# Kernel optimization log

Hardware: AMD Instinct MI355X
Metric: run time of the kernel (lower is better)

## Reference

```python
import jax, jax.numpy as jnp
import numpy as np

EPS = 1e-4          # module eps
GROUPS = 8
N_POWER_ITERS = 19  # fixed iteration count for power_iteration_unstable


def _l2n(v):
    return v / (jnp.linalg.norm(v) + 1e-12)


def _whiten_subspace(A, v_init):
    """Sequential power iteration + deflation on one LxL covariance block.
    A: (L, L), v_init: (L, L) random start vectors (one per eigen-index).
    Returns whitening subspace (L, L). Early-exit (break) emulated with a
    'stopped' flag carried through lax.scan."""
    L = A.shape[0]

    def step(carry, inputs):
        A, subspace, lam_prev, stopped = carry
        j, v0 = inputs
        v = _l2n(v0)

        def pi(v, _):
            return _l2n(A @ v), None
        v, _ = jax.lax.scan(pi, v, None, length=N_POWER_ITERS)

        Av = A @ v
        lam = (v @ Av) / (v @ v)          # Rayleigh quotient
        brk = (j > 0) & ((lam_prev < lam) | (lam < EPS))  # torch break condition
        active = (~stopped) & (~brk)
        lam_safe = jnp.where(active, lam, 1.0)
        vvT = jnp.outer(v, v)
        subspace = subspace + jnp.where(active, jax.lax.rsqrt(lam_safe), 0.0) * vvT
        A = jnp.where(active, A - A @ vvT, A)
        lam_prev = jnp.where(active, lam, lam_prev)
        stopped = stopped | brk
        return (A, subspace, lam_prev, stopped), None

    init = (A, jnp.zeros_like(A), jnp.zeros((), A.dtype), jnp.zeros((), bool))
    (_, subspace, _, _), _ = jax.lax.scan(step, init, (jnp.arange(L), v_init))
    return subspace


def setup_inputs() -> dict:
    key = jax.random.key(0)
    k1, k2, k3 = jax.random.split(key, 3)
    N, C, H, W = 32, 512, 56, 56
    L = C // GROUPS
    x = jax.random.normal(k1, (N, C, H, W), dtype=jnp.float32)
    v_init = jax.random.normal(k2, (GROUPS, L, L), dtype=jnp.float32)
    weight = jax.random.uniform(k3, (C, 1), dtype=jnp.float32)
    bias = jnp.zeros((C, 1), dtype=jnp.float32)
    return {"x": x, "v_init": v_init, "weight": weight, "bias": bias}


def reference(x, v_init, weight, bias):
    N, C, H, W = x.shape
    G = GROUPS
    L = C // G
    M = N * H * W
    xc = x.transpose(1, 0, 2, 3).reshape(C, M)        # (C, M)
    mu = xc.mean(axis=1, keepdims=True)
    xc = xc - mu
    xg = xc.reshape(G, L, M)                           # per-group channels
    # diagonal blocks of (x x^T)/M + eps*I
    cov = jnp.einsum('gim,gjm->gij', xg, xg) / M + EPS * jnp.eye(L, dtype=xc.dtype)
    subspaces = jax.vmap(_whiten_subspace)(cov, v_init)  # (G, L, L)
    xgr = jnp.einsum('gij,gjm->gim', subspaces, xg)      # whitened
    xr = xgr.reshape(C, M) * weight + bias               # affine
    return xr.reshape(C, N, H, W).transpose(1, 0, 2, 3)
```

## Files before the change

kernel.cpp:

```cpp
#include <hip/hip_runtime.h>
#include <math.h>

#define EPSV 1e-4f
#define NG 8
#define LL 64
#define NB 32
#define CC 512
#define HWS 3136
#define MTOT (NB * HWS)
#define NPI 19
#define NTILES 49
#define NPW 4

template <int CTRL>
__device__ __forceinline__ float dpp_add(float v) {
  int x = __builtin_amdgcn_update_dpp(0, __float_as_int(v), CTRL, 0xF, 0xF, true);
  return v + __int_as_float(x);
}

__device__ __forceinline__ float wave_allsum(float v) {
  v = dpp_add<0xB1>(v);
  v = dpp_add<0x4E>(v);
  v = dpp_add<0x141>(v);
  v = dpp_add<0x140>(v);
  v += __int_as_float(__builtin_amdgcn_ds_swizzle(__float_as_int(v), 0x401F));
  v += __shfl_xor(v, 32, 64);
  return v;
}

__global__ __launch_bounds__(256, 2) void k_moments(const float* __restrict__ x,
                                                    float* __restrict__ prods,
                                                    float* __restrict__ sums,
                                                    int nparts) {
  const int g = blockIdx.x, n = blockIdx.y, h = blockIdx.z;
  const int tid = threadIdx.x;
  const int q = tid >> 6, l = tid & 63;
  const int ty = tid >> 4, tx = tid & 15;
  __shared__ float xs[64][68];
  const float* xp = x + ((size_t)(n * CC + g * LL)) * HWS;

  float acc[4][4];
#pragma unroll
  for (int a = 0; a < 4; ++a)
#pragma unroll
    for (int b = 0; b < 4; ++b) acc[a][b] = 0.f;
  float csum[16];
#pragma unroll
  for (int r = 0; r < 16; ++r) csum[r] = 0.f;

  const int tpp = (NTILES + nparts - 1) / nparts;
  const int t0 = h * tpp;
  const int t1 = (t0 + tpp < NTILES) ? (t0 + tpp) : NTILES;

  for (int t = t0; t < t1; ++t) {
    const int hw0 = t * 64;
    __syncthreads();
#pragma unroll
    for (int r = 0; r < 16; ++r) {
      const int ch = r * 4 + q;
      float v = xp[ch * HWS + hw0 + l];
      xs[l][ch] = v;
      csum[r] += v;
    }
    __syncthreads();
#pragma unroll 4
    for (int mm = 0; mm < 64; ++mm) {
      const float4* row = (const float4*)(&xs[mm][0]);
      float4 av = row[ty];
      float4 bv = row[tx];
      float a4[4] = {av.x, av.y, av.z, av.w};
      float b4[4] = {bv.x, bv.y, bv.z, bv.w};
#pragma unroll
      for (int ii = 0; ii < 4; ++ii)
#pragma unroll
        for (int jj = 0; jj < 4; ++jj) acc[ii][jj] += a4[ii] * b4[jj];
    }
  }

  const int p = n * nparts + h;
  float* pp = prods + ((size_t)(g * NB * nparts + p)) * 4096;
#pragma unroll
  for (int ii = 0; ii < 4; ++ii) {
    *(float4*)&pp[(ty * 4 + ii) * 64 + tx * 4] =
        make_float4(acc[ii][0], acc[ii][1], acc[ii][2], acc[ii][3]);
  }
#pragma unroll
  for (int r = 0; r < 16; ++r) {
    float s = wave_allsum(csum[r]);
    if (l == 0) sums[((size_t)(g * NB * nparts + p)) * 64 + r * 4 + q] = s;
  }
}

__global__ __launch_bounds__(64) void k_mu(const float* __restrict__ sums,
                                           float* __restrict__ mu, int P) {
  const int g = blockIdx.x;
  const int tid = threadIdx.x;
  const float* sp = sums + (size_t)g * P * 64 + tid;
  float s0 = 0.f, s1 = 0.f, s2 = 0.f, s3 = 0.f;
  int p = 0;
  for (; p + 4 <= P; p += 4) {
    s0 += sp[(size_t)(p + 0) * 64];
    s1 += sp[(size_t)(p + 1) * 64];
    s2 += sp[(size_t)(p + 2) * 64];
    s3 += sp[(size_t)(p + 3) * 64];
  }
  for (; p < P; ++p) s0 += sp[(size_t)p * 64];
  mu[g * 64 + tid] = ((s0 + s1) + (s2 + s3)) / (float)MTOT;
}

__global__ __launch_bounds__(256) void k_cov(const float* __restrict__ prods,
                                             const float* __restrict__ mu,
                                             float* __restrict__ cov, int P) {
  const int g = blockIdx.x;
  const int e = blockIdx.y * 256 + threadIdx.x;
  const int i = e >> 6, j = e & 63;
  const float* pp = prods + (size_t)g * P * 4096 + e;
  float s0 = 0.f, s1 = 0.f, s2 = 0.f, s3 = 0.f;
  int p = 0;
  for (; p + 4 <= P; p += 4) {
    s0 += pp[(size_t)(p + 0) * 4096];
    s1 += pp[(size_t)(p + 1) * 4096];
    s2 += pp[(size_t)(p + 2) * 4096];
    s3 += pp[(size_t)(p + 3) * 4096];
  }
  for (; p < P; ++p) s0 += pp[(size_t)p * 4096];
  const float s = (s0 + s1) + (s2 + s3);
  const float cv =
      s / (float)MTOT - mu[g * 64 + i] * mu[g * 64 + j] + (i == j ? EPSV : 0.f);
  cov[(size_t)g * 4096 + e] = cv;
}

__device__ __forceinline__ float dot64(const float* Arow, const float* v_sh) {
  float d0 = 0.f, d1 = 0.f, d2 = 0.f, d3 = 0.f;
#pragma unroll
  for (int c4 = 0; c4 < 16; ++c4) {
    float4 vv = ((const float4*)v_sh)[c4];
    d0 += Arow[c4 * 4 + 0] * vv.x;
    d1 += Arow[c4 * 4 + 1] * vv.y;
    d2 += Arow[c4 * 4 + 2] * vv.z;
    d3 += Arow[c4 * 4 + 3] * vv.w;
  }
  return (d0 + d1) + (d2 + d3);
}

__global__ __launch_bounds__(64, 1) void k_power(const float* __restrict__ v_init,
                                                 const float* __restrict__ cov,
                                                 float* __restrict__ sub) {
  const int g = blockIdx.x;
  const int r = threadIdx.x;
  __shared__ __align__(16) float v_sh[64];
  float Arow[64], Srow[64];
  const float4* crow = (const float4*)(cov + (size_t)g * 4096 + r * 64);
#pragma unroll
  for (int c4 = 0; c4 < 16; ++c4) {
    float4 cv = crow[c4];
    Arow[c4 * 4 + 0] = cv.x;
    Arow[c4 * 4 + 1] = cv.y;
    Arow[c4 * 4 + 2] = cv.z;
    Arow[c4 * 4 + 3] = cv.w;
    Srow[c4 * 4 + 0] = 0.f;
    Srow[c4 * 4 + 1] = 0.f;
    Srow[c4 * 4 + 2] = 0.f;
    Srow[c4 * 4 + 3] = 0.f;
  }

  float lam_prev = 0.f;
  for (int j = 0; j < 64; ++j) {
    float v0 = v_init[((size_t)g * 64 + j) * 64 + r];
    float ss = wave_allsum(v0 * v0);
    float vr = v0 / (sqrtf(ss) + 1e-12f);
    __syncthreads();
    v_sh[r] = vr;
    __syncthreads();

    for (int it = 0; it < NPI; ++it) {
      float w = dot64(Arow, v_sh);
      float s2 = wave_allsum(w * w);
      vr = w / (sqrtf(s2) + 1e-12f);
      __syncthreads();
      v_sh[r] = vr;
      __syncthreads();
    }

    const float Avr = dot64(Arow, v_sh);
    const float num = wave_allsum(vr * Avr);
    const float den = wave_allsum(vr * vr);
    const float lam = num / den;

    if (j > 0 && (lam_prev < lam || lam < EPSV)) break;

    const float sc = 1.f / sqrtf(lam);
    const float svr = sc * vr;
#pragma unroll
    for (int c4 = 0; c4 < 16; ++c4) {
      float4 vv = ((const float4*)v_sh)[c4];
      Srow[c4 * 4 + 0] += svr * vv.x;
      Srow[c4 * 4 + 1] += svr * vv.y;
      Srow[c4 * 4 + 2] += svr * vv.z;
      Srow[c4 * 4 + 3] += svr * vv.w;
      Arow[c4 * 4 + 0] -= Avr * vv.x;
      Arow[c4 * 4 + 1] -= Avr * vv.y;
      Arow[c4 * 4 + 2] -= Avr * vv.z;
      Arow[c4 * 4 + 3] -= Avr * vv.w;
    }
    lam_prev = lam;
  }

  float4* srow = (float4*)(sub + (size_t)g * 4096 + r * 64);
#pragma unroll
  for (int c4 = 0; c4 < 16; ++c4)
    srow[c4] = make_float4(Srow[c4 * 4 + 0], Srow[c4 * 4 + 1], Srow[c4 * 4 + 2],
                           Srow[c4 * 4 + 3]);
}

__global__ __launch_bounds__(256, 2) void k_whiten(const float* __restrict__ x,
                                                   const float* __restrict__ weight,
                                                   const float* __restrict__ bias,
                                                   const float* __restrict__ mu,
                                                   const float* __restrict__ sub,
                                                   float* __restrict__ out,
                                                   int nparts) {
  const int g = blockIdx.x, n = blockIdx.y, h = blockIdx.z;
  const int tid = threadIdx.x;
  const int q = tid >> 6, l = tid & 63;
  const int ty = tid >> 4, tx = tid & 15;
  __shared__ float xs[64][68];
  __shared__ float ST[64][68];
  __shared__ float mu_sh[64];

  const float* sp = sub + (size_t)g * 4096;
#pragma unroll
  for (int r = 0; r < 16; ++r) {
    const int i = r * 4 + q;
    ST[l][i] = sp[i * 64 + l];
  }
  if (tid < 64) mu_sh[tid] = mu[g * 64 + tid];

  float wgt[4], bs[4];
#pragma unroll
  for (int ii = 0; ii < 4; ++ii) {
    const int cch = g * LL + ty * 4 + ii;
    wgt[ii] = weight[cch];
    bs[ii] = bias[cch];
  }

  const float* xp = x + ((size_t)(n * CC + g * LL)) * HWS;
  float* yp = out + ((size_t)(n * CC + g * LL)) * HWS;
  const int tpp = (NTILES + nparts - 1) / nparts;
  const int t0 = h * tpp;
  const int t1 = (t0 + tpp < NTILES) ? (t0 + tpp) : NTILES;

  __syncthreads();
  for (int t = t0; t < t1; ++t) {
    const int hw0 = t * 64;
    if (t > t0) __syncthreads();
#pragma unroll
    for (int r = 0; r < 16; ++r) {
      const int ch = r * 4 + q;
      xs[ch][l] = xp[ch * HWS + hw0 + l] - mu_sh[ch];
    }
    __syncthreads();

    float acc[4][4];
#pragma unroll
    for (int ii = 0; ii < 4; ++ii)
#pragma unroll
      for (int jj = 0; jj < 4; ++jj) acc[ii][jj] = 0.f;

#pragma unroll 4
    for (int j = 0; j < 64; ++j) {
      float4 sv = ((const float4*)(&ST[j][0]))[ty];
      float4 xv = ((const float4*)(&xs[j][0]))[tx];
      float s4[4] = {sv.x, sv.y, sv.z, sv.w};
      float x4[4] = {xv.x, xv.y, xv.z, xv.w};
#pragma unroll
      for (int ii = 0; ii < 4; ++ii)
#pragma unroll
        for (int jj = 0; jj < 4; ++jj) acc[ii][jj] += s4[ii] * x4[jj];
    }

#pragma unroll
    for (int ii = 0; ii < 4; ++ii) {
      float4 o;
      o.x = acc[ii][0] * wgt[ii] + bs[ii];
      o.y = acc[ii][1] * wgt[ii] + bs[ii];
      o.z = acc[ii][2] * wgt[ii] + bs[ii];
      o.w = acc[ii][3] * wgt[ii] + bs[ii];
      *(float4*)&yp[(ty * 4 + ii) * HWS + hw0 + tx * 4] = o;
    }
  }
}

extern "C" void kernel_launch(void* const* d_in, const int* in_sizes, int n_in,
                              void* d_out, int out_size, void* d_ws, size_t ws_size,
                              hipStream_t stream) {
  const float* x = (const float*)d_in[0];
  const float* v_init = (const float*)d_in[1];
  const float* weight = (const float*)d_in[2];
  const float* bias = (const float*)d_in[3];
  float* out = (float*)d_out;
  float* ws = (float*)d_ws;

  const size_t fixed = (size_t)512 + (size_t)2 * NG * 4096;
  auto need = [&](int np) {
    return ((size_t)NG * NB * np * (4096 + 64) + fixed) * sizeof(float);
  };
  int nparts = 7;
  if (ws_size < need(nparts)) nparts = 4;
  if (ws_size < need(nparts)) nparts = 2;
  if (ws_size < need(nparts)) nparts = 1;

  const int P = NB * nparts;
  float* prods = ws;
  float* sums = prods + (size_t)NG * P * 64;
  sums = prods + (size_t)NG * P * 4096;
  float* mu = sums + (size_t)NG * P * 64;
  float* cov = mu + 512;
  float* sub = cov + (size_t)NG * 4096;

  k_moments<<<dim3(NG, NB, nparts), 256, 0, stream>>>(x, prods, sums, nparts);
  k_mu<<<NG, 64, 0, stream>>>(sums, mu, P);
  k_cov<<<dim3(NG, 16), 256, 0, stream>>>(prods, mu, cov, P);
  k_power<<<NG, 64, 0, stream>>>(v_init, cov, sub);
  k_whiten<<<dim3(NG, NB, NPW), 256, 0, stream>>>(x, weight, bias, mu, sub, out, NPW);
}
```

Before: 510.7 us.

## Use 8x8 register tiles, float4 loads, and mean folding in moments/whiten kernels

```diff
diff --git a/kernel.cpp b/kernel.cpp
--- a/kernel.cpp
+++ b/kernel.cpp
@@ -10,40 +10,48 @@
 #define MTOT (NB * HWS)
 #define NPI 19
 #define NTILES 49
-#define NPW 4
-
-template <int CTRL>
-__device__ __forceinline__ float dpp_add(float v) {
-  int x = __builtin_amdgcn_update_dpp(0, __float_as_int(v), CTRL, 0xF, 0xF, true);
+#define NPW 3
+
+template <int CTRL, int RMASK, bool BC>
+__device__ __forceinline__ float dpp_fadd(float v) {
+  int x = __builtin_amdgcn_update_dpp(0, __float_as_int(v), CTRL, RMASK, 0xF, BC);
   return v + __int_as_float(x);
 }
 
 __device__ __forceinline__ float wave_allsum(float v) {
-  v = dpp_add<0xB1>(v);
-  v = dpp_add<0x4E>(v);
-  v = dpp_add<0x141>(v);
-  v = dpp_add<0x140>(v);
-  v += __int_as_float(__builtin_amdgcn_ds_swizzle(__float_as_int(v), 0x401F));
-  v += __shfl_xor(v, 32, 64);
+  v = dpp_fadd<0x111, 0xF, true>(v);
+  v = dpp_fadd<0x112, 0xF, true>(v);
+  v = dpp_fadd<0x114, 0xF, true>(v);
+  v = dpp_fadd<0x118, 0xF, true>(v);
+  v = dpp_fadd<0x142, 0xa, false>(v);
+  v = dpp_fadd<0x143, 0xc, false>(v);
+  return __int_as_float(__builtin_amdgcn_readlane(__float_as_int(v), 63));
+}
+
+__device__ __forceinline__ float row16_sum(float v) {
+  v = dpp_fadd<0x111, 0xF, true>(v);
+  v = dpp_fadd<0x112, 0xF, true>(v);
+  v = dpp_fadd<0x114, 0xF, true>(v);
+  v = dpp_fadd<0x118, 0xF, true>(v);
   return v;
 }
 
-__global__ __launch_bounds__(256, 2) void k_moments(const float* __restrict__ x,
-                                                    float* __restrict__ prods,
-                                                    float* __restrict__ sums,
-                                                    int nparts) {
+__global__ __launch_bounds__(64, 2) void k_moments(const float* __restrict__ x,
+                                                   float* __restrict__ prods,
+                                                   float* __restrict__ sums,
+                                                   int nparts) {
   const int g = blockIdx.x, n = blockIdx.y, h = blockIdx.z;
-  const int tid = threadIdx.x;
-  const int q = tid >> 6, l = tid & 63;
-  const int ty = tid >> 4, tx = tid & 15;
-  __shared__ float xs[64][68];
+  const int l = threadIdx.x;
+  const int c = l >> 4, m4w = l & 15;
+  const int ty = l >> 3, tx = l & 7;
+  __shared__ float xs[64 * 64];
   const float* xp = x + ((size_t)(n * CC + g * LL)) * HWS;
 
-  float acc[4][4];
-#pragma unroll
-  for (int a = 0; a < 4; ++a)
-#pragma unroll
-    for (int b = 0; b < 4; ++b) acc[a][b] = 0.f;
+  float acc[8][8];
+#pragma unroll
+  for (int a = 0; a < 8; ++a)
+#pragma unroll
+    for (int b = 0; b < 8; ++b) acc[a][b] = 0.f;
   float csum[16];
 #pragma unroll
   for (int r = 0; r < 16; ++r) csum[r] = 0.f;
@@ -57,37 +65,47 @@
     __syncthreads();
 #pragma unroll
     for (int r = 0; r < 16; ++r) {
-      const int ch = r * 4 + q;
-      float v = xp[ch * HWS + hw0 + l];
-      xs[l][ch] = v;
-      csum[r] += v;
-    }
-    __syncthreads();
-#pragma unroll 4
-    for (int mm = 0; mm < 64; ++mm) {
-      const float4* row = (const float4*)(&xs[mm][0]);
-      float4 av = row[ty];
-      float4 bv = row[tx];
-      float a4[4] = {av.x, av.y, av.z, av.w};
-      float b4[4] = {bv.x, bv.y, bv.z, bv.w};
-#pragma unroll
-      for (int ii = 0; ii < 4; ++ii)
-#pragma unroll
-        for (int jj = 0; jj < 4; ++jj) acc[ii][jj] += a4[ii] * b4[jj];
+      const int ch = r * 4 + c;
+      float4 gv = *(const float4*)&xp[ch * HWS + hw0 + m4w * 4];
+      csum[r] += (gv.x + gv.y) + (gv.z + gv.w);
+      const int slot = m4w ^ (ch >> 3);
+      *(float4*)&xs[ch * 64 + slot * 4] = gv;
+    }
+    __syncthreads();
+#pragma unroll 2
+    for (int m4 = 0; m4 < 16; ++m4) {
+      float4 av[8], bv[8];
+#pragma unroll
+      for (int ii = 0; ii < 8; ++ii)
+        av[ii] = *(const float4*)&xs[(ty * 8 + ii) * 64 + ((m4 ^ ty) * 4)];
+#pragma unroll
+      for (int jj = 0; jj < 8; ++jj)
+        bv[jj] = *(const float4*)&xs[(tx * 8 + jj) * 64 + ((m4 ^ tx) * 4)];
+#pragma unroll
+      for (int ii = 0; ii < 8; ++ii)
+#pragma unroll
+        for (int jj = 0; jj < 8; ++jj) {
+          acc[ii][jj] += av[ii].x * bv[jj].x;
+          acc[ii][jj] += av[ii].y * bv[jj].y;
+          acc[ii][jj] += av[ii].z * bv[jj].z;
+          acc[ii][jj] += av[ii].w * bv[jj].w;
+        }
     }
   }
 
   const int p = n * nparts + h;
   float* pp = prods + ((size_t)(g * NB * nparts + p)) * 4096;
 #pragma unroll
-  for (int ii = 0; ii < 4; ++ii) {
-    *(float4*)&pp[(ty * 4 + ii) * 64 + tx * 4] =
+  for (int ii = 0; ii < 8; ++ii) {
+    *(float4*)&pp[(ty * 8 + ii) * 64 + tx * 8] =
         make_float4(acc[ii][0], acc[ii][1], acc[ii][2], acc[ii][3]);
+    *(float4*)&pp[(ty * 8 + ii) * 64 + tx * 8 + 4] =
+        make_float4(acc[ii][4], acc[ii][5], acc[ii][6], acc[ii][7]);
   }
 #pragma unroll
   for (int r = 0; r < 16; ++r) {
-    float s = wave_allsum(csum[r]);
-    if (l == 0) sums[((size_t)(g * NB * nparts + p)) * 64 + r * 4 + q] = s;
+    float s = row16_sum(csum[r]);
+    if (m4w == 15) sums[((size_t)(g * NB * nparts + p)) * 64 + r * 4 + c] = s;
   }
 }
 
@@ -213,7 +231,7 @@
                            Srow[c4 * 4 + 3]);
 }
 
-__global__ __launch_bounds__(256, 2) void k_whiten(const float* __restrict__ x,
+__global__ __launch_bounds__(128, 2) void k_whiten(const float* __restrict__ x,
                                                    const float* __restrict__ weight,
                                                    const float* __restrict__ bias,
                                                    const float* __restrict__ mu,
@@ -222,26 +240,39 @@
                                                    int nparts) {
   const int g = blockIdx.x, n = blockIdx.y, h = blockIdx.z;
   const int tid = threadIdx.x;
-  const int q = tid >> 6, l = tid & 63;
-  const int ty = tid >> 4, tx = tid & 15;
-  __shared__ float xs[64][68];
-  __shared__ float ST[64][68];
+  const int w = tid >> 6, l = tid & 63;
+  const int c = l >> 4, m4w = l & 15;
+  const int ty = l >> 3, tx = l & 7;
+  __shared__ float SS[64][68];
+  __shared__ float xsb[2][64 * 64];
   __shared__ float mu_sh[64];
+  float* xs = xsb[w];
 
   const float* sp = sub + (size_t)g * 4096;
-#pragma unroll
-  for (int r = 0; r < 16; ++r) {
-    const int i = r * 4 + q;
-    ST[l][i] = sp[i * 64 + l];
-  }
+  for (int i = w * 32; i < w * 32 + 32; ++i) SS[l][i] = sp[i * 64 + l];
   if (tid < 64) mu_sh[tid] = mu[g * 64 + tid];
 
-  float wgt[4], bs[4];
-#pragma unroll
-  for (int ii = 0; ii < 4; ++ii) {
-    const int cch = g * LL + ty * 4 + ii;
+  float wgt[8], bs[8];
+#pragma unroll
+  for (int ii = 0; ii < 8; ++ii) {
+    const int cch = g * LL + ty * 8 + ii;
     wgt[ii] = weight[cch];
     bs[ii] = bias[cch];
+  }
+  __syncthreads();
+
+  float smu[8];
+#pragma unroll
+  for (int ii = 0; ii < 8; ++ii) smu[ii] = 0.f;
+#pragma unroll 4
+  for (int j = 0; j < 64; ++j) {
+    const float mj = mu_sh[j];
+    float4 s0 = *(const float4*)&SS[j][ty * 8];
+    float4 s1 = *(const float4*)&SS[j][ty * 8 + 4];
+    smu[0] += s0.x * mj; smu[1] += s0.y * mj;
+    smu[2] += s0.z * mj; smu[3] += s0.w * mj;
+    smu[4] += s1.x * mj; smu[5] += s1.y * mj;
+    smu[6] += s1.z * mj; smu[7] += s1.w * mj;
   }
 
   const float* xp = x + ((size_t)(n * CC + g * LL)) * HWS;
@@ -249,44 +280,58 @@
   const int tpp = (NTILES + nparts - 1) / nparts;
   const int t0 = h * tpp;
   const int t1 = (t0 + tpp < NTILES) ? (t0 + tpp) : NTILES;
-
-  __syncthreads();
-  for (int t = t0; t < t1; ++t) {
+  const int nt = t1 - t0;
+  const int rounds = (nt + 1) >> 1;
+
+  for (int rr = 0; rr < rounds; ++rr) {
+    const int t = t0 + rr * 2 + w;
+    const bool act = t < t1;
     const int hw0 = t * 64;
-    if (t > t0) __syncthreads();
-#pragma unroll
-    for (int r = 0; r < 16; ++r) {
-      const int ch = r * 4 + q;
-      xs[ch][l] = xp[ch * HWS + hw0 + l] - mu_sh[ch];
-    }
-    __syncthreads();
-
-    float acc[4][4];
-#pragma unroll
-    for (int ii = 0; ii < 4; ++ii)
-#pragma unroll
-      for (int jj = 0; jj < 4; ++jj) acc[ii][jj] = 0.f;
+    __syncthreads();
+    if (act) {
+#pragma unroll
+      for (int r = 0; r < 16; ++r) {
+        const int ch = r * 4 + c;
+        float4 gv = *(const float4*)&xp[ch * HWS + hw0 + m4w * 4];
+        *(float4*)&xs[ch * 64 + m4w * 4] = gv;
+      }
+    }
+    __syncthreads();
+    if (!act) continue;
+
+    float acc[8][8];
+#pragma unroll
+    for (int ii = 0; ii < 8; ++ii)
+#pragma unroll
+      for (int jj = 0; jj < 8; ++jj) acc[ii][jj] = 0.f;
 
 #pragma unroll 4
     for (int j = 0; j < 64; ++j) {
-      float4 sv = ((const float4*)(&ST[j][0]))[ty];
-      float4 xv = ((const float4*)(&xs[j][0]))[tx];
-      float s4[4] = {sv.x, sv.y, sv.z, sv.w};
-      float x4[4] = {xv.x, xv.y, xv.z, xv.w};
-#pragma unroll
-      for (int ii = 0; ii < 4; ++ii)
-#pragma unroll
-        for (int jj = 0; jj < 4; ++jj) acc[ii][jj] += s4[ii] * x4[jj];
-    }
-
-#pragma unroll
-    for (int ii = 0; ii < 4; ++ii) {
-      float4 o;
-      o.x = acc[ii][0] * wgt[ii] + bs[ii];
-      o.y = acc[ii][1] * wgt[ii] + bs[ii];
-      o.z = acc[ii][2] * wgt[ii] + bs[ii];
-      o.w = acc[ii][3] * wgt[ii] + bs[ii];
-      *(float4*)&yp[(ty * 4 + ii) * HWS + hw0 + tx * 4] = o;
+      float4 s0 = *(const float4*)&SS[j][ty * 8];
+      float4 s1 = *(const float4*)&SS[j][ty * 8 + 4];
+      float4 x0 = *(const float4*)&xs[j * 64 + tx * 8];
+      float4 x1 = *(const float4*)&xs[j * 64 + tx * 8 + 4];
+      float sv[8] = {s0.x, s0.y, s0.z, s0.w, s1.x, s1.y, s1.z, s1.w};
+      float xv[8] = {x0.x, x0.y, x0.z, x0.w, x1.x, x1.y, x1.z, x1.w};
+#pragma unroll
+      for (int ii = 0; ii < 8; ++ii)
+#pragma unroll
+        for (int jj = 0; jj < 8; ++jj) acc[ii][jj] += sv[ii] * xv[jj];
+    }
+
+#pragma unroll
+    for (int ii = 0; ii < 8; ++ii) {
+      float4 o0, o1;
+      o0.x = (acc[ii][0] - smu[ii]) * wgt[ii] + bs[ii];
+      o0.y = (acc[ii][1] - smu[ii]) * wgt[ii] + bs[ii];
+      o0.z = (acc[ii][2] - smu[ii]) * wgt[ii] + bs[ii];
+      o0.w = (acc[ii][3] - smu[ii]) * wgt[ii] + bs[ii];
+      o1.x = (acc[ii][4] - smu[ii]) * wgt[ii] + bs[ii];
+      o1.y = (acc[ii][5] - smu[ii]) * wgt[ii] + bs[ii];
+      o1.z = (acc[ii][6] - smu[ii]) * wgt[ii] + bs[ii];
+      o1.w = (acc[ii][7] - smu[ii]) * wgt[ii] + bs[ii];
+      *(float4*)&yp[(ty * 8 + ii) * HWS + hw0 + tx * 8] = o0;
+      *(float4*)&yp[(ty * 8 + ii) * HWS + hw0 + tx * 8 + 4] = o1;
     }
   }
 }
@@ -312,15 +357,14 @@
 
   const int P = NB * nparts;
   float* prods = ws;
-  float* sums = prods + (size_t)NG * P * 64;
-  sums = prods + (size_t)NG * P * 4096;
+  float* sums = prods + (size_t)NG * P * 4096;
   float* mu = sums + (size_t)NG * P * 64;
   float* cov = mu + 512;
   float* sub = cov + (size_t)NG * 4096;
 
-  k_moments<<<dim3(NG, NB, nparts), 256, 0, stream>>>(x, prods, sums, nparts);
+  k_moments<<<dim3(NG, NB, nparts), 64, 0, stream>>>(x, prods, sums, nparts);
   k_mu<<<NG, 64, 0, stream>>>(sums, mu, P);
   k_cov<<<dim3(NG, 16), 256, 0, stream>>>(prods, mu, cov, P);
   k_power<<<NG, 64, 0, stream>>>(v_init, cov, sub);
-  k_whiten<<<dim3(NG, NB, NPW), 256, 0, stream>>>(x, weight, bias, mu, sub, out, NPW);
-}
+  k_whiten<<<dim3(NG, NB, NPW), 128, 0, stream>>>(x, weight, bias, mu, sub, out, NPW);
+}
```

Result: slower. 531.4 us (+4.0%).
